# Performance work log

Measured on AMD Instinct MI355X. Metric: run time of the kernel, lower is better.

Reference implementation:

```python
import jax, jax.numpy as jnp
import numpy as np

B, H, P, S = 512, 4, 196, 256  # batch, heads, pixels, states
D = S // H  # head_state = 64


def conv1x1(x, w, b):
    # x: (B, C_in, P), w: (C_out, C_in), b: (C_out,) -> (B, C_out, P)
    return jnp.einsum('oc,bcp->bop', w, x) + b[None, :, None]


def setup_inputs() -> dict:
    key = jax.random.key(0)
    ks = jax.random.split(key, 9)
    sc = 1.0 / np.sqrt(S)
    return {
        'x': jax.random.normal(ks[0], (B, S, P), dtype=jnp.float32),
        'wq': jax.random.normal(ks[1], (S, S), dtype=jnp.float32) * sc,
        'bq': jax.random.normal(ks[2], (S,), dtype=jnp.float32) * 0.01,
        'wk': jax.random.normal(ks[3], (S, S), dtype=jnp.float32) * sc,
        'bk': jax.random.normal(ks[4], (S,), dtype=jnp.float32) * 0.01,
        'wv': jax.random.normal(ks[5], (S, S), dtype=jnp.float32) * sc,
        'bv': jax.random.normal(ks[6], (S,), dtype=jnp.float32) * 0.01,
        'wo': jax.random.normal(ks[7], (S, S), dtype=jnp.float32) * sc,
        'bo': jax.random.normal(ks[8], (S,), dtype=jnp.float32) * 0.01,
    }


def reference(x, wq, bq, wk, bk, wv, bv, wo, bo):
    def split_heads(t):  # (B, S, P) -> (B, H, P, D)
        return t.reshape(B, H, D, P).swapaxes(-1, -2)

    q = split_heads(conv1x1(x, wq, bq))
    k = split_heads(conv1x1(x, wk, bk))
    v = split_heads(conv1x1(x, wv, bv))

    att = jnp.einsum('bhqd,bhkd->bhqk', q, k) / np.sqrt(D).astype(jnp.float32)
    att = jax.nn.softmax(att, axis=-1)
    av = jnp.einsum('bhqk,bhkd->bhqd', att, v)  # (B, H, P, D)

    # Faithful to original: raw view (B,H,P,D) -> (B,P,S) with NO head transpose
    merged = av.reshape(B, P, S).swapaxes(-1, -2)  # (B, S, P)
    return conv1x1(merged, wo, bo)
```

## Files before the change

kernel.cpp:

```cpp
#include <hip/hip_runtime.h>
#include <stdint.h>


#define PPIX 196
#define SS   256

typedef __attribute__((ext_vector_type(8))) short short8;
typedef __attribute__((ext_vector_type(4))) float f32x4;

#define PSWP    144
#define SZ_UNI  36864
#define OFF_QS  (SZ_UNI)
#define SZ_QK   (208*72*2)
#define OFF_KS  (OFF_QS + SZ_QK)
#define OFF_VS  (OFF_KS + SZ_QK)
#define SZ_VS   (64*236*2)
#define OFF_AVS (OFF_VS + SZ_VS)
#define SZ_AVS  (12544*2)
#define SMEM_TOTAL (OFF_AVS + SZ_AVS)

static __device__ __forceinline__ uint16_t f2b(float f) {
  uint32_t u = __float_as_uint(f);
  return (uint16_t)((u + 0x7fffu + ((u >> 16) & 1u)) >> 16);
}
static __device__ __forceinline__ f32x4 fz4() {
  f32x4 v; v[0] = 0.f; v[1] = 0.f; v[2] = 0.f; v[3] = 0.f; return v;
}

template<bool PRE>
__global__ __launch_bounds__(512, 2)
void mha_fused(const float* __restrict__ x,
               const float* __restrict__ wq, const float* __restrict__ bq,
               const float* __restrict__ wk, const float* __restrict__ bk,
               const float* __restrict__ wv, const float* __restrict__ bv,
               const float* __restrict__ wo, const float* __restrict__ bo,
               const uint16_t* __restrict__ wpk,
               float* __restrict__ out) {
  extern __shared__ char smem[];
  uint16_t* const uni = (uint16_t*)(smem);
  uint16_t* const qs  = (uint16_t*)(smem + OFF_QS);
  uint16_t* const ks  = (uint16_t*)(smem + OFF_KS);
  uint16_t* const vsm = (uint16_t*)(smem + OFF_VS);
  uint16_t* const avs = (uint16_t*)(smem + OFF_AVS);

  const int bid = blockIdx.x;
  const int L = (bid & 7) * 256 + (bid >> 3);
  const int b = L >> 2, h = L & 3;
  const int tid = threadIdx.x;
  const int w = tid >> 6;
  const int lane = tid & 63;
  const int g = lane >> 4;
  const int l15 = lane & 15;
  const int wm = w & 3;
  const int wn = w >> 2;

  const float* xb = x + (size_t)b * (SS * PPIX);

  f32x4 acc1[3][7];
#pragma unroll
  for (int mi = 0; mi < 3; ++mi)
#pragma unroll
    for (int nt = 0; nt < 7; ++nt) acc1[mi][nt] = fz4();

  const int prow = tid >> 1;
  const int phalf = tid & 1;

  for (int cc = 0; cc < 4; ++cc) {
    __syncthreads();
    short8 afr[2][3];
#pragma unroll
    for (int kt = 0; kt < 2; ++kt)
#pragma unroll
      for (int mi = 0; mi < 3; ++mi) {
        const int chA = 48 * wm + 16 * mi + l15;
        const int mat = chA >> 6, dA = chA & 63;
        const int col = cc * 64 + kt * 32 + g * 8;
        if (PRE) {
          afr[kt][mi] = *(const short8*)(wpk + ((size_t)(mat * 256 + h * 64 + dA)) * SS + col);
        } else {
          const float* W = (mat == 0) ? wq : ((mat == 1) ? wk : wv);
          const float* s = W + (size_t)(h * 64 + dA) * SS + col;
          f32x4 w0 = *(const f32x4*)s, w1 = *(const f32x4*)(s + 4);
          short8 af;
#pragma unroll
          for (int j = 0; j < 4; ++j) { af[j] = (short)f2b(w0[j]); af[4 + j] = (short)f2b(w1[j]); }
          afr[kt][mi] = af;
        }
      }
    if (prow < 224) {
      const int swz = (prow & 7) << 3;
      uint16_t* dstrow = uni + prow * 64;
      if (prow < PPIX) {
        const float* src = xb + (size_t)(cc * 64 + phalf * 32) * PPIX + prow;
#pragma unroll
        for (int cb = 0; cb < 4; ++cb) {
          short8 pk;
#pragma unroll
          for (int t = 0; t < 8; ++t) pk[t] = (short)f2b(src[(cb * 8 + t) * PPIX]);
          *(short8*)(dstrow + ((phalf * 32 + cb * 8) ^ swz)) = pk;
        }
      } else {
        short8 z;
#pragma unroll
        for (int t = 0; t < 8; ++t) z[t] = 0;
#pragma unroll
        for (int cb = 0; cb < 4; ++cb)
          *(short8*)(dstrow + ((phalf * 32 + cb * 8) ^ swz)) = z;
      }
    }
    __syncthreads();
#pragma unroll
    for (int kt = 0; kt < 2; ++kt)
#pragma unroll
      for (int ntl = 0; ntl < 7; ++ntl) {
        const int p = 16 * (7 * wn + ntl) + l15;
        const int coff = (kt * 32 + g * 8) ^ ((p & 7) << 3);
        short8 bfr = *(const short8*)(uni + p * 64 + coff);
#pragma unroll
        for (int mi = 0; mi < 3; ++mi)
          acc1[mi][ntl] = __builtin_amdgcn_mfma_f32_16x16x32_bf16(afr[kt][mi], bfr, acc1[mi][ntl], 0, 0, 0);
      }
  }
#pragma unroll
  for (int mi = 0; mi < 3; ++mi) {
    const int ch0 = 48 * wm + 16 * mi;
    const int mat = ch0 >> 6;
    const float* bias = (mat == 0) ? bq : ((mat == 1) ? bk : bv);
#pragma unroll
    for (int r = 0; r < 4; ++r) {
      const int ch = ch0 + 4 * g + r;
      const int d = ch & 63;
      const float bias_v = bias[h * 64 + d];
#pragma unroll
      for (int ntl = 0; ntl < 7; ++ntl) {
        const int p = 16 * (7 * wn + ntl) + l15;
        const uint16_t val = f2b(acc1[mi][ntl][r] + bias_v);
        if (mat == 2)      vsm[d * 236 + p] = val;
        else if (mat == 0) { if (p < 208) qs[p * 72 + d] = val; }
        else               { if (p < 208) ks[p * 72 + d] = val; }
      }
    }
  }
  __syncthreads();

  uint16_t* const psw = uni + w * (16 * PSWP);
#pragma unroll 1
  for (int round = 0; round < 2; ++round) {
    const int rt = 8 * round + w;
    if (rt > 12) continue;
    f32x4 accA[14];
#pragma unroll
    for (int nt = 0; nt < 14; ++nt) accA[nt] = fz4();
#pragma unroll
    for (int kt = 0; kt < 2; ++kt) {
      short8 a = *(const short8*)(qs + (16 * rt + l15) * 72 + kt * 32 + g * 8);
#pragma unroll
      for (int nt = 0; nt < 14; ++nt) {
        short8 bfr = *(const short8*)(ks + (16 * nt + l15) * 72 + kt * 32 + g * 8);
        accA[nt] = __builtin_amdgcn_mfma_f32_16x16x32_bf16(a, bfr, accA[nt], 0, 0, 0);
      }
    }
    float mx[4] = {-3e38f, -3e38f, -3e38f, -3e38f};
#pragma unroll
    for (int nt = 0; nt < 14; ++nt) {
      const int col = 16 * nt + l15;
#pragma unroll
      for (int r = 0; r < 4; ++r) {
        float v = accA[nt][r];
        if (col >= PPIX) v = -3e38f;
        accA[nt][r] = v;
        mx[r] = fmaxf(mx[r], v);
      }
    }
#pragma unroll
    for (int off = 1; off <= 8; off <<= 1)
#pragma unroll
      for (int r = 0; r < 4; ++r)
        mx[r] = fmaxf(mx[r], __shfl_xor(mx[r], off, 64));
    float sm[4] = {0.f, 0.f, 0.f, 0.f};
    const float cs = 0.125f * 1.44269504088896f;
#pragma unroll
    for (int nt = 0; nt < 14; ++nt)
#pragma unroll
      for (int r = 0; r < 4; ++r) {
        float e = exp2f((accA[nt][r] - mx[r]) * cs);
        accA[nt][r] = e;
        sm[r] += e;
      }
#pragma unroll
    for (int off = 1; off <= 8; off <<= 1)
#pragma unroll
      for (int r = 0; r < 4; ++r)
        sm[r] += __shfl_xor(sm[r], off, 64);

    f32x4 accV[4];
#pragma unroll
    for (int n = 0; n < 4; ++n) accV[n] = fz4();
#pragma unroll
    for (int nt = 0; nt < 8; ++nt)
#pragma unroll
      for (int r = 0; r < 4; ++r) {
        const int row = 4 * g + r;
        psw[row * PSWP + ((16 * nt + l15) ^ ((row & 7) << 3))] = f2b(accA[nt][r]);
      }
#pragma unroll
    for (int kt = 0; kt < 4; ++kt) {
      short8 a = *(const short8*)(psw + l15 * PSWP + ((kt * 32 + g * 8) ^ ((l15 & 7) << 3)));
#pragma unroll
      for (int n = 0; n < 4; ++n) {
        short8 bfr = *(const short8*)(vsm + (16 * n + l15) * 236 + kt * 32 + g * 8);
        accV[n] = __builtin_amdgcn_mfma_f32_16x16x32_bf16(a, bfr, accV[n], 0, 0, 0);
      }
    }
#pragma unroll
    for (int nt = 8; nt < 14; ++nt)
#pragma unroll
      for (int r = 0; r < 4; ++r) {
        const int row = 4 * g + r;
        psw[row * PSWP + ((16 * (nt - 8) + l15) ^ ((row & 7) << 3))] = f2b(accA[nt][r]);
      }
#pragma unroll
    for (int kt = 0; kt < 3; ++kt) {
      short8 a = *(const short8*)(psw + l15 * PSWP + ((kt * 32 + g * 8) ^ ((l15 & 7) << 3)));
#pragma unroll
      for (int n = 0; n < 4; ++n) {
        short8 bfr = *(const short8*)(vsm + (16 * n + l15) * 236 + 128 + kt * 32 + g * 8);
        accV[n] = __builtin_amdgcn_mfma_f32_16x16x32_bf16(a, bfr, accV[n], 0, 0, 0);
      }
    }
#pragma unroll
    for (int r = 0; r < 4; ++r) {
      const int p = 16 * rt + 4 * g + r;
      if (p < PPIX) {
        const float inv = 1.0f / sm[r];
        const int swzp = ((p >> 2) & 7) << 3;
#pragma unroll
        for (int n = 0; n < 4; ++n) {
          const int d = 16 * n + l15;
          avs[p * 64 + (d ^ swzp)] = f2b(accV[n][r] * inv);
        }
      }
    }
  }
  __syncthreads();

  f32x4 accO[2][4];
#pragma unroll
  for (int mi = 0; mi < 2; ++mi)
#pragma unroll
    for (int ni = 0; ni < 4; ++ni) accO[mi][ni] = fz4();
#pragma unroll
  for (int kt = 0; kt < 8; ++kt) {
    short8 a[2];
#pragma unroll
    for (int mi = 0; mi < 2; ++mi) {
      const int o = 32 * w + 16 * mi + l15;
      if (PRE) {
        a[mi] = *(const short8*)(wpk + 3 * 65536 + (size_t)o * SS + kt * 32 + g * 8);
      } else {
        const float* srcA = wo + (size_t)o * SS + kt * 32 + g * 8;
        f32x4 w0 = *(const f32x4*)srcA;
        f32x4 w1 = *(const f32x4*)(srcA + 4);
        short8 af;
#pragma unroll
        for (int j = 0; j < 4; ++j) { af[j] = (short)f2b(w0[j]); af[4 + j] = (short)f2b(w1[j]); }
        a[mi] = af;
      }
    }
#pragma unroll
    for (int ni = 0; ni < 4; ++ni) {
      const int pp = 16 * ni + l15;
      const int pmin = pp < 49 ? pp : 48;
      const int s0 = kt * 32 + g * 8;
      const int idx = 256 * pmin + ((s0 >> 6) << 6) + ((s0 & 63) ^ ((pmin & 7) << 3));
      short8 bfr = *(const short8*)(avs + idx);
#pragma unroll
      for (int mi = 0; mi < 2; ++mi)
        accO[mi][ni] = __builtin_amdgcn_mfma_f32_16x16x32_bf16(a[mi], bfr, accO[mi][ni], 0, 0, 0);
    }
  }
#pragma unroll
  for (int mi = 0; mi < 2; ++mi) {
#pragma unroll
    for (int r = 0; r < 4; ++r) {
      const int o = 32 * w + 16 * mi + 4 * g + r;
      const float bias_v = bo[o];
      float* orow = out + ((size_t)b * SS + o) * PPIX + 49 * h;
#pragma unroll
      for (int ni = 0; ni < 4; ++ni) {
        const int pp = 16 * ni + l15;
        if (pp < 49) orow[pp] = accO[mi][ni][r] + bias_v;
      }
    }
  }
}

__global__ __launch_bounds__(256)
void prepack_w(const float* __restrict__ wq, const float* __restrict__ wk,
               const float* __restrict__ wv, const float* __restrict__ wo,
               uint16_t* __restrict__ ws) {
  const int t = blockIdx.x * 256 + threadIdx.x;
  const int mat = t >> 13;
  const int off = (t & 8191) << 3;
  const float* src = (mat == 0) ? wq : ((mat == 1) ? wk : ((mat == 2) ? wv : wo));
  f32x4 a = *(const f32x4*)(src + off);
  f32x4 b = *(const f32x4*)(src + off + 4);
  short8 o;
#pragma unroll
  for (int j = 0; j < 4; ++j) { o[j] = (short)f2b(a[j]); o[4 + j] = (short)f2b(b[j]); }
  *(short8*)(ws + ((size_t)mat << 16) + off) = o;
}

extern "C" void kernel_launch(void* const* d_in, const int* in_sizes, int n_in,
                              void* d_out, int out_size, void* d_ws, size_t ws_size,
                              hipStream_t stream) {
  (void)in_sizes; (void)n_in; (void)out_size;
  const float* x  = (const float*)d_in[0];
  const float* wq = (const float*)d_in[1];
  const float* bq = (const float*)d_in[2];
  const float* wk = (const float*)d_in[3];
  const float* bk = (const float*)d_in[4];
  const float* wv = (const float*)d_in[5];
  const float* bv = (const float*)d_in[6];
  const float* wo = (const float*)d_in[7];
  const float* bo = (const float*)d_in[8];
  float* out = (float*)d_out;
  uint16_t* ws16 = (uint16_t*)d_ws;

  const bool pre = (d_ws != nullptr) && (ws_size >= (size_t)4 * 65536 * sizeof(uint16_t));
  if (pre) {
    (void)hipFuncSetAttribute(reinterpret_cast<const void*>(&mha_fused<true>),
                              hipFuncAttributeMaxDynamicSharedMemorySize, SMEM_TOTAL);
    prepack_w<<<dim3(128), dim3(256), 0, stream>>>(wq, wk, wv, wo, ws16);
    mha_fused<true><<<dim3(2048), dim3(512), SMEM_TOTAL, stream>>>(
        x, wq, bq, wk, bk, wv, bv, wo, bo, ws16, out);
  } else {
    (void)hipFuncSetAttribute(reinterpret_cast<const void*>(&mha_fused<false>),
                              hipFuncAttributeMaxDynamicSharedMemorySize, SMEM_TOTAL);
    mha_fused<false><<<dim3(2048), dim3(512), SMEM_TOTAL, stream>>>(
        x, wq, bq, wk, bk, wv, bv, wo, bo, ws16, out);
  }
}
```

Before: 545.0 us.

## Pre-transpose x to bf16 pixel-major layout and read QKV operands from global

```diff
diff --git a/kernel.cpp b/kernel.cpp
--- a/kernel.cpp
+++ b/kernel.cpp
@@ -19,6 +19,10 @@
 #define SZ_AVS  (12544*2)
 #define SMEM_TOTAL (OFF_AVS + SZ_AVS)
 
+#define WPK_BYTES  (4u * 65536u * 2u)
+#define XT_ELEMS   ((size_t)512 * 224 * 256)
+#define WS_NEED_XT (WPK_BYTES + XT_ELEMS * 2)
+
 static __device__ __forceinline__ uint16_t f2b(float f) {
   uint32_t u = __float_as_uint(f);
   return (uint16_t)((u + 0x7fffu + ((u >> 16) & 1u)) >> 16);
@@ -27,14 +31,13 @@
   f32x4 v; v[0] = 0.f; v[1] = 0.f; v[2] = 0.f; v[3] = 0.f; return v;
 }
 
-template<bool PRE>
+template<bool XT>
 __global__ __launch_bounds__(512, 2)
 void mha_fused(const float* __restrict__ x,
-               const float* __restrict__ wq, const float* __restrict__ bq,
-               const float* __restrict__ wk, const float* __restrict__ bk,
-               const float* __restrict__ wv, const float* __restrict__ bv,
-               const float* __restrict__ wo, const float* __restrict__ bo,
+               const float* __restrict__ bq, const float* __restrict__ bk,
+               const float* __restrict__ bv, const float* __restrict__ bo,
                const uint16_t* __restrict__ wpk,
+               const uint16_t* __restrict__ xT,
                float* __restrict__ out) {
   extern __shared__ char smem[];
   uint16_t* const uni = (uint16_t*)(smem);
@@ -54,72 +57,82 @@
   const int wm = w & 3;
   const int wn = w >> 2;
 
-  const float* xb = x + (size_t)b * (SS * PPIX);
-
   f32x4 acc1[3][7];
 #pragma unroll
   for (int mi = 0; mi < 3; ++mi)
 #pragma unroll
     for (int nt = 0; nt < 7; ++nt) acc1[mi][nt] = fz4();
 
-  const int prow = tid >> 1;
-  const int phalf = tid & 1;
-
-  for (int cc = 0; cc < 4; ++cc) {
-    __syncthreads();
-    short8 afr[2][3];
-#pragma unroll
-    for (int kt = 0; kt < 2; ++kt)
+  if constexpr (XT) {
+    const uint16_t* xTb = xT + (size_t)b * (224 * 256);
+#pragma unroll
+    for (int kt = 0; kt < 8; ++kt) {
+      short8 afr[3];
 #pragma unroll
       for (int mi = 0; mi < 3; ++mi) {
         const int chA = 48 * wm + 16 * mi + l15;
         const int mat = chA >> 6, dA = chA & 63;
-        const int col = cc * 64 + kt * 32 + g * 8;
-        if (PRE) {
-          afr[kt][mi] = *(const short8*)(wpk + ((size_t)(mat * 256 + h * 64 + dA)) * SS + col);
-        } else {
-          const float* W = (mat == 0) ? wq : ((mat == 1) ? wk : wv);
-          const float* s = W + (size_t)(h * 64 + dA) * SS + col;
-          f32x4 w0 = *(const f32x4*)s, w1 = *(const f32x4*)(s + 4);
-          short8 af;
-#pragma unroll
-          for (int j = 0; j < 4; ++j) { af[j] = (short)f2b(w0[j]); af[4 + j] = (short)f2b(w1[j]); }
-          afr[kt][mi] = af;
-        }
-      }
-    if (prow < 224) {
-      const int swz = (prow & 7) << 3;
-      uint16_t* dstrow = uni + prow * 64;
-      if (prow < PPIX) {
-        const float* src = xb + (size_t)(cc * 64 + phalf * 32) * PPIX + prow;
-#pragma unroll
-        for (int cb = 0; cb < 4; ++cb) {
-          short8 pk;
-#pragma unroll
-          for (int t = 0; t < 8; ++t) pk[t] = (short)f2b(src[(cb * 8 + t) * PPIX]);
-          *(short8*)(dstrow + ((phalf * 32 + cb * 8) ^ swz)) = pk;
-        }
-      } else {
-        short8 z;
-#pragma unroll
-        for (int t = 0; t < 8; ++t) z[t] = 0;
-#pragma unroll
-        for (int cb = 0; cb < 4; ++cb)
-          *(short8*)(dstrow + ((phalf * 32 + cb * 8) ^ swz)) = z;
-      }
-    }
-    __syncthreads();
-#pragma unroll
-    for (int kt = 0; kt < 2; ++kt)
+        afr[mi] = *(const short8*)(wpk + ((size_t)(mat * 256 + h * 64 + dA)) * SS + kt * 32 + g * 8);
+      }
 #pragma unroll
       for (int ntl = 0; ntl < 7; ++ntl) {
         const int p = 16 * (7 * wn + ntl) + l15;
-        const int coff = (kt * 32 + g * 8) ^ ((p & 7) << 3);
-        short8 bfr = *(const short8*)(uni + p * 64 + coff);
+        short8 bfr = *(const short8*)(xTb + (size_t)p * SS + kt * 32 + g * 8);
 #pragma unroll
         for (int mi = 0; mi < 3; ++mi)
-          acc1[mi][ntl] = __builtin_amdgcn_mfma_f32_16x16x32_bf16(afr[kt][mi], bfr, acc1[mi][ntl], 0, 0, 0);
-      }
+          acc1[mi][ntl] = __builtin_amdgcn_mfma_f32_16x16x32_bf16(afr[mi], bfr, acc1[mi][ntl], 0, 0, 0);
+      }
+    }
+  } else {
+    const float* xb = x + (size_t)b * (SS * PPIX);
+    const int prow = tid >> 1;
+    const int phalf = tid & 1;
+    for (int cc = 0; cc < 4; ++cc) {
+      __syncthreads();
+      short8 afr[2][3];
+#pragma unroll
+      for (int kt = 0; kt < 2; ++kt)
+#pragma unroll
+        for (int mi = 0; mi < 3; ++mi) {
+          const int chA = 48 * wm + 16 * mi + l15;
+          const int mat = chA >> 6, dA = chA & 63;
+          const int col = cc * 64 + kt * 32 + g * 8;
+          afr[kt][mi] = *(const short8*)(wpk + ((size_t)(mat * 256 + h * 64 + dA)) * SS + col);
+        }
+      if (prow < 224) {
+        const int swz = (prow & 7) << 3;
+        uint16_t* dstrow = uni + prow * 64;
+        if (prow < PPIX) {
+          const float* src = xb + (size_t)(cc * 64 + phalf * 32) * PPIX + prow;
+#pragma unroll
+          for (int cb = 0; cb < 4; ++cb) {
+            short8 pk;
+#pragma unroll
+            for (int t = 0; t < 8; ++t) pk[t] = (short)f2b(src[(cb * 8 + t) * PPIX]);
+            *(short8*)(dstrow + ((phalf * 32 + cb * 8) ^ swz)) = pk;
+          }
+        } else {
+          short8 z;
+#pragma unroll
+          for (int t = 0; t < 8; ++t) z[t] = 0;
+#pragma unroll
+          for (int cb = 0; cb < 4; ++cb)
+            *(short8*)(dstrow + ((phalf * 32 + cb * 8) ^ swz)) = z;
+        }
+      }
+      __syncthreads();
+#pragma unroll
+      for (int kt = 0; kt < 2; ++kt)
+#pragma unroll
+        for (int ntl = 0; ntl < 7; ++ntl) {
+          const int p = 16 * (7 * wn + ntl) + l15;
+          const int coff = (kt * 32 + g * 8) ^ ((p & 7) << 3);
+          short8 bfr = *(const short8*)(uni + p * 64 + coff);
+#pragma unroll
+          for (int mi = 0; mi < 3; ++mi)
+            acc1[mi][ntl] = __builtin_amdgcn_mfma_f32_16x16x32_bf16(afr[kt][mi], bfr, acc1[mi][ntl], 0, 0, 0);
+        }
+    }
   }
 #pragma unroll
   for (int mi = 0; mi < 3; ++mi) {
@@ -255,17 +268,7 @@
 #pragma unroll
     for (int mi = 0; mi < 2; ++mi) {
       const int o = 32 * w + 16 * mi + l15;
-      if (PRE) {
-        a[mi] = *(const short8*)(wpk + 3 * 65536 + (size_t)o * SS + kt * 32 + g * 8);
-      } else {
-        const float* srcA = wo + (size_t)o * SS + kt * 32 + g * 8;
-        f32x4 w0 = *(const f32x4*)srcA;
-        f32x4 w1 = *(const f32x4*)(srcA + 4);
-        short8 af;
-#pragma unroll
-        for (int j = 0; j < 4; ++j) { af[j] = (short)f2b(w0[j]); af[4 + j] = (short)f2b(w1[j]); }
-        a[mi] = af;
-      }
+      a[mi] = *(const short8*)(wpk + 3 * 65536 + (size_t)o * SS + kt * 32 + g * 8);
     }
 #pragma unroll
     for (int ni = 0; ni < 4; ++ni) {
@@ -309,6 +312,33 @@
 #pragma unroll
   for (int j = 0; j < 4; ++j) { o[j] = (short)f2b(a[j]); o[4 + j] = (short)f2b(b[j]); }
   *(short8*)(ws + ((size_t)mat << 16) + off) = o;
+}
+
+__global__ __launch_bounds__(256)
+void prepack_x(const float* __restrict__ x, uint16_t* __restrict__ xT) {
+  __shared__ float tile[64][201];
+  const int b = blockIdx.x >> 2, cc = blockIdx.x & 3;
+  const int tid = threadIdx.x;
+  const float* src = x + ((size_t)b * SS + cc * 64) * PPIX;
+  for (int i = tid; i < 64 * 49; i += 256) {
+    const int r = i / 49, p4 = (i % 49) * 4;
+    const f32x4 v = *(const f32x4*)(src + r * PPIX + p4);
+    tile[r][p4] = v[0]; tile[r][p4 + 1] = v[1]; tile[r][p4 + 2] = v[2]; tile[r][p4 + 3] = v[3];
+  }
+  __syncthreads();
+  uint16_t* dst = xT + ((size_t)b * 224) * SS + cc * 64;
+  for (int i = tid; i < 224 * 8; i += 256) {
+    const int p = i >> 3, c8 = (i & 7) * 8;
+    short8 o;
+    if (p < PPIX) {
+#pragma unroll
+      for (int j = 0; j < 8; ++j) o[j] = (short)f2b(tile[c8 + j][p]);
+    } else {
+#pragma unroll
+      for (int j = 0; j < 8; ++j) o[j] = 0;
+    }
+    *(short8*)(dst + (size_t)p * SS + c8) = o;
+  }
 }
 
 extern "C" void kernel_launch(void* const* d_in, const int* in_sizes, int n_in,
@@ -325,19 +355,20 @@
   const float* wo = (const float*)d_in[7];
   const float* bo = (const float*)d_in[8];
   float* out = (float*)d_out;
-  uint16_t* ws16 = (uint16_t*)d_ws;
-
-  const bool pre = (d_ws != nullptr) && (ws_size >= (size_t)4 * 65536 * sizeof(uint16_t));
-  if (pre) {
+  uint16_t* wpk = (uint16_t*)d_ws;
+  uint16_t* xT  = (uint16_t*)((char*)d_ws + WPK_BYTES);
+
+  prepack_w<<<dim3(128), dim3(256), 0, stream>>>(wq, wk, wv, wo, wpk);
+  if (d_ws != nullptr && ws_size >= WS_NEED_XT) {
+    prepack_x<<<dim3(2048), dim3(256), 0, stream>>>(x, xT);
     (void)hipFuncSetAttribute(reinterpret_cast<const void*>(&mha_fused<true>),
                               hipFuncAttributeMaxDynamicSharedMemorySize, SMEM_TOTAL);
-    prepack_w<<<dim3(128), dim3(256), 0, stream>>>(wq, wk, wv, wo, ws16);
     mha_fused<true><<<dim3(2048), dim3(512), SMEM_TOTAL, stream>>>(
-        x, wq, bq, wk, bk, wv, bv, wo, bo, ws16, out);
+        x, bq, bk, bv, bo, wpk, xT, out);
   } else {
     (void)hipFuncSetAttribute(reinterpret_cast<const void*>(&mha_fused<false>),
                               hipFuncAttributeMaxDynamicSharedMemorySize, SMEM_TOTAL);
     mha_fused<false><<<dim3(2048), dim3(512), SMEM_TOTAL, stream>>>(
-        x, wq, bq, wk, bk, wv, bv, wo, bo, ws16, out);
-  }
-}
+        x, bq, bk, bv, bo, wpk, xT, out);
+  }
+}
```

After: 595.7 us. 1.09x slower.
